# Optimization experiments

Measured on AMD Instinct MI355X. Metric: run time of the kernel, lower is better.

## Reference

```python
import jax, jax.numpy as jnp
import numpy as np

C = 128
K = 5
M = 150000   # num vertices
NF = 300000  # num faces
D = 192      # volume side
NEG_SLOPE = 0.2


def _x_shift(K):
    # Exactly replicates the torch module's grid construction.
    grid = np.linspace(-K // 2, K // 2, K)
    grid_3d = np.stack(np.meshgrid(grid, grid, grid), axis=0).transpose(2, 1, 3, 0)
    return jnp.asarray(grid_3d.reshape(-1, 3), jnp.float32)  # [K^3, 3]


def _trilinear_border(vol, g):
    # vol: [D1, D2, D3]; g: [N, 3] normalized coords in (x, y, z) order
    # (x -> D3/W, y -> D2/H, z -> D1/D), align_corners=True, padding_mode='border'.
    D1, D2, D3 = vol.shape
    def pix(c, S):
        return jnp.clip((c + 1.0) * 0.5 * (S - 1), 0.0, S - 1.0)
    ix, iy, iz = pix(g[:, 0], D3), pix(g[:, 1], D2), pix(g[:, 2], D1)
    x0f, y0f, z0f = jnp.floor(ix), jnp.floor(iy), jnp.floor(iz)
    wx, wy, wz = ix - x0f, iy - y0f, iz - z0f
    x0 = x0f.astype(jnp.int32); y0 = y0f.astype(jnp.int32); z0 = z0f.astype(jnp.int32)
    x1 = jnp.minimum(x0 + 1, D3 - 1)
    y1 = jnp.minimum(y0 + 1, D2 - 1)
    z1 = jnp.minimum(z0 + 1, D1 - 1)
    c000 = vol[z0, y0, x0]; c001 = vol[z0, y0, x1]
    c010 = vol[z0, y1, x0]; c011 = vol[z0, y1, x1]
    c100 = vol[z1, y0, x0]; c101 = vol[z1, y0, x1]
    c110 = vol[z1, y1, x0]; c111 = vol[z1, y1, x1]
    c00 = c000 * (1 - wx) + c001 * wx
    c01 = c010 * (1 - wx) + c011 * wx
    c10 = c100 * (1 - wx) + c101 * wx
    c11 = c110 * (1 - wx) + c111 * wx
    c0 = c00 * (1 - wy) + c01 * wy
    c1 = c10 * (1 - wy) + c11 * wy
    return c0 * (1 - wz) + c1 * wz


def _leaky(x):
    return jnp.where(x >= 0, x, NEG_SLOPE * x)


def setup_inputs() -> dict:
    key = jax.random.key(0)
    ks = jax.random.split(key, 9)
    v = jax.random.uniform(ks[0], (1, M, 3), jnp.float32, -0.9, 0.9)
    f = jax.random.randint(ks[1], (1, NF, 3), 0, M, jnp.int32)
    V = jax.random.normal(ks[2], (1, 1, D, D, D), jnp.float32)
    def init(k, shape, fan):
        return jax.random.normal(k, shape, jnp.float32) / np.sqrt(fan).astype(np.float32)
    Wconv = init(ks[3], (C, 1, K, K, K), K ** 3)
    bconv = jnp.zeros((C,), jnp.float32)
    Wlfc = init(ks[4], (C, C), C)
    blfc = jnp.zeros((C,), jnp.float32)
    W1 = init(ks[5], (C, 6), 6)
    b1 = jnp.zeros((C,), jnp.float32)
    W2 = init(ks[6], (4 * C, 2 * C), 2 * C)
    b2 = jnp.zeros((4 * C,), jnp.float32)
    W3 = init(ks[7], (2 * C, 4 * C), 4 * C)
    b3 = jnp.zeros((2 * C,), jnp.float32)
    return dict(v=v, f=f, V=V, Wconv=Wconv, bconv=bconv, Wlfc=Wlfc, blfc=blfc,
                W1=W1, b1=b1, W2=W2, b2=b2, W3=W3, b3=b3)


def reference(v, f, V, Wconv, bconv, Wlfc, blfc, W1, b1, W2, b2, W3, b3):
    m = v.shape[1]
    D1, D2, D3 = V.shape[2], V.shape[3], V.shape[4]
    Dm = max(D1, D2, D3)
    rescale = jnp.array([D3 / Dm, D2 / Dm, D1 / Dm], jnp.float32)
    x_shift = _x_shift(K)  # [K^3, 3]

    # --- cube sampling (Q = n_scale = 1), done under no_grad in torch ---
    pts = (v[0][:, None, :] + x_shift / Dm * 2.0) / rescale  # [m, K^3, 3]
    cubes = _trilinear_border(V[0, 0], pts.reshape(-1, 3)).reshape(m, K ** 3)
    cubes = jax.lax.stop_gradient(cubes)

    # --- localconv: Conv3d with full-size kernel == GEMM over flattened cube ---
    z_local = cubes @ Wconv.reshape(C, -1).T + bconv      # [m, C]
    z_local = _leaky(z_local)
    z_local = _leaky(z_local @ Wlfc.T + blfc)             # [m, C]

    # --- vertex normals (area-weighted face-normal accumulation, pytorch3d style) ---
    faces = f[0]
    vv = v[0]
    p0, p1, p2 = vv[faces[:, 0]], vv[faces[:, 1]], vv[faces[:, 2]]
    fn = jnp.cross(p1 - p0, p2 - p0)
    vn = jnp.zeros_like(vv)
    vn = vn.at[faces[:, 0]].add(fn).at[faces[:, 1]].add(fn).at[faces[:, 2]].add(fn)
    vn = vn / jnp.maximum(jnp.linalg.norm(vn, axis=-1, keepdims=True), 1e-6)

    # --- point-wise MLP fusion ---
    x = jnp.concatenate([v, vn[None]], axis=2)            # [1, m, 6]
    z_point = _leaky(x @ W1.T + b1)                       # [1, m, C]
    z = jnp.concatenate([z_point, z_local[None]], axis=2) # [1, m, 2C]
    z = _leaky(z @ W2.T + b2)                             # [1, m, 4C]
    z = _leaky(z @ W3.T + b3)                             # [1, m, 2C]
    return z
```

## Files before the change

kernel.cpp:

```cpp
#include <hip/hip_runtime.h>
#include <hip/hip_fp16.h>

#define NEG_SLOPE 0.2f

using f16x8 = __attribute__((ext_vector_type(8))) _Float16;
using f32x4 = __attribute__((ext_vector_type(4))) float;

__device__ __forceinline__ float leakyf(float x) { return x >= 0.f ? x : NEG_SLOPE * x; }

__device__ __forceinline__ void gload_lds16(const void* g, void* l) {
    __builtin_amdgcn_global_load_lds(
        (const __attribute__((address_space(1))) unsigned int*)g,
        (__attribute__((address_space(3))) unsigned int*)l, 16, 0, 0);
}

#define MFMA16(a, b, c) __builtin_amdgcn_mfma_f32_16x16x32_f16(a, b, c, 0, 0, 0)

__global__ __launch_bounds__(256)
void fn_kernel(const float* __restrict__ v, const int* __restrict__ f,
               float4* __restrict__ fn4, int nf) {
    int i = blockIdx.x * 256 + threadIdx.x;
    if (i >= nf) return;
    int i0 = f[3 * i], i1 = f[3 * i + 1], i2 = f[3 * i + 2];
    float p0x = v[3 * i0], p0y = v[3 * i0 + 1], p0z = v[3 * i0 + 2];
    float ux = v[3 * i1] - p0x, uy = v[3 * i1 + 1] - p0y, uz = v[3 * i1 + 2] - p0z;
    float wx = v[3 * i2] - p0x, wy = v[3 * i2 + 1] - p0y, wz = v[3 * i2 + 2] - p0z;
    fn4[i] = make_float4(uy * wz - uz * wy, uz * wx - ux * wz, ux * wy - uy * wx, 0.f);
}

__global__ __launch_bounds__(256)
void inc_hist_kernel(const int* __restrict__ f, unsigned* __restrict__ gh, int NE) {
    __shared__ unsigned h[1024];
    const int t = threadIdx.x, blk = blockIdx.x;
    h[t] = 0; h[t + 256] = 0; h[t + 512] = 0; h[t + 768] = 0;
    __syncthreads();
    int base = blk * 4096;
#pragma unroll
    for (int k = 0; k < 16; ++k) {
        int idx = base + k * 256 + t;
        if (idx < NE) atomicAdd(&h[((unsigned)f[idx]) >> 8], 1u);
    }
    __syncthreads();
#pragma unroll
    for (int k = 0; k < 4; ++k) { int b = t + k * 256; gh[(size_t)blk * 1024 + b] = h[b]; }
}

__global__ __launch_bounds__(256)
void row_scan_kernel(unsigned* __restrict__ gh, unsigned* __restrict__ binTotals, int NB) {
    __shared__ unsigned s[256];
    __shared__ unsigned carrySh;
    const int bin = blockIdx.x, t = threadIdx.x;
    if (t == 0) carrySh = 0;
    __syncthreads();
    for (int base = 0; base < NB; base += 256) {
        unsigned c = carrySh;
        int i = base + t;
        unsigned val = (i < NB) ? gh[(size_t)i * 1024 + bin] : 0;
        s[t] = val;
        __syncthreads();
        for (int d = 1; d < 256; d <<= 1) {
            unsigned x = (t >= d) ? s[t - d] : 0;
            __syncthreads();
            s[t] += x;
            __syncthreads();
        }
        if (i < NB) gh[(size_t)i * 1024 + bin] = s[t] - val + c;
        if (t == 255) carrySh = c + s[255];
        __syncthreads();
    }
    if (t == 0) binTotals[bin] = carrySh;
}

__global__ __launch_bounds__(1024)
void bin_scan_kernel(const unsigned* __restrict__ binTotals, unsigned* __restrict__ binstart) {
    __shared__ unsigned s[1024];
    int t = threadIdx.x;
    unsigned val = binTotals[t];
    s[t] = val;
    __syncthreads();
    for (int d = 1; d < 1024; d <<= 1) {
        unsigned x = (t >= d) ? s[t - d] : 0;
        __syncthreads();
        s[t] += x;
        __syncthreads();
    }
    binstart[t] = s[t] - val;
    if (t == 1023) binstart[1024] = s[1023];
}

__global__ __launch_bounds__(256)
void inc_scatter_kernel(const int* __restrict__ f, const unsigned* __restrict__ gh,
                        const unsigned* __restrict__ binstart,
                        unsigned* __restrict__ sortedV, unsigned* __restrict__ sortedE,
                        int NE) {
    __shared__ unsigned loc[1024];
    const int t = threadIdx.x, blk = blockIdx.x;
#pragma unroll
    for (int k = 0; k < 4; ++k) {
        int b = t + k * 256;
        loc[b] = gh[(size_t)blk * 1024 + b] + binstart[b];
    }
    __syncthreads();
    int base = blk * 4096;
#pragma unroll
    for (int k = 0; k < 16; ++k) {
        int idx = base + k * 256 + t;
        if (idx < NE) {
            unsigned vv = (unsigned)f[idx];
            unsigned pos = atomicAdd(&loc[vv >> 8], 1u);
            sortedV[pos] = vv;
            sortedE[pos] = (unsigned)idx;
        }
    }
}

__global__ __launch_bounds__(256)
void vn_gather_kernel(const unsigned* __restrict__ sortedV, const unsigned* __restrict__ sortedE,
                      const float4* __restrict__ fn4, const unsigned* __restrict__ binstart,
                      float* __restrict__ vn, int M) {
    __shared__ float acc[768];
    const int t = threadIdx.x, b = blockIdx.x;
    acc[t] = 0.f; acc[t + 256] = 0.f; acc[t + 512] = 0.f;
    __syncthreads();
    unsigned s = binstart[b], e = binstart[b + 1];
    for (unsigned i = s + t; i < e; i += 256) {
        unsigned vv = sortedV[i];
        float4 fn = fn4[sortedE[i] / 3];
        int lv = (int)(vv & 255u) * 3;
        atomicAdd(&acc[lv + 0], fn.x);
        atomicAdd(&acc[lv + 1], fn.y);
        atomicAdd(&acc[lv + 2], fn.z);
    }
    __syncthreads();
    int gv = b * 256 + t;
    if (gv < M) {
        vn[3 * gv + 0] = acc[t * 3 + 0];
        vn[3 * gv + 1] = acc[t * 3 + 1];
        vn[3 * gv + 2] = acc[t * 3 + 2];
    }
}

__global__ __launch_bounds__(256)
void code_hist_kernel(const float* __restrict__ v, int* __restrict__ codes,
                      int* __restrict__ hist, int M) {
    int i = blockIdx.x * 256 + threadIdx.x;
    if (i >= M) return;
    int cx = min(max((int)((v[3 * i + 0] + 1.f) * 8.f), 0), 15);
    int cy = min(max((int)((v[3 * i + 1] + 1.f) * 8.f), 0), 15);
    int cz = min(max((int)((v[3 * i + 2] + 1.f) * 8.f), 0), 15);
    int code = 0;
#pragma unroll
    for (int b = 0; b < 4; ++b)
        code |= (((cx >> b) & 1) << (3 * b)) | (((cy >> b) & 1) << (3 * b + 1)) |
                (((cz >> b) & 1) << (3 * b + 2));
    codes[i] = code;
    atomicAdd(&hist[code], 1);
}

__global__ __launch_bounds__(1024)
void scan_kernel(const int* __restrict__ hist, int* __restrict__ offs) {
    __shared__ int s[1024];
    int t = threadIdx.x;
    int v0 = hist[4 * t], v1 = hist[4 * t + 1], v2 = hist[4 * t + 2], v3 = hist[4 * t + 3];
    int sum = v0 + v1 + v2 + v3;
    s[t] = sum;
    __syncthreads();
    for (int d = 1; d < 1024; d <<= 1) {
        int val = (t >= d) ? s[t - d] : 0;
        __syncthreads();
        s[t] += val;
        __syncthreads();
    }
    int excl = s[t] - sum;
    offs[4 * t + 0] = excl;
    offs[4 * t + 1] = excl + v0;
    offs[4 * t + 2] = excl + v0 + v1;
    offs[4 * t + 3] = excl + v0 + v1 + v2;
}

__global__ __launch_bounds__(256)
void scatter_kernel(const int* __restrict__ codes, int* __restrict__ offs,
                    int* __restrict__ perm, int M) {
    int i = blockIdx.x * 256 + threadIdx.x;
    if (i >= M) return;
    int pos = atomicAdd(&offs[codes[i]], 1);
    perm[pos] = i;
}

__global__ __launch_bounds__(256)
void sample_kernel(const float* __restrict__ v, const float* __restrict__ vol,
                   const int* __restrict__ perm,
                   __half* __restrict__ cubes, int m_start, int cnt, int nwg) {
    __shared__ float bbox[2][448];
    __shared__ int pi0[2][16];
    __shared__ float pw[2][16];
    const int half = threadIdx.x >> 7;
    const int q = threadIdx.x & 127;
    int q8 = nwg >> 3, r8 = nwg & 7;
    int xcd = blockIdx.x & 7, idxb = blockIdx.x >> 3;
    int bid = (xcd < r8 ? xcd * (q8 + 1) : r8 * (q8 + 1) + (xcd - r8) * q8) + idxb;
    int ml = bid * 2 + half;
    bool valid = ml < cnt;
    int m = valid ? perm[m_start + ml] : 0;

    if (valid && q < 15) {
        int axis = q / 5, idx = q - 5 * axis;
        float g = -3.f + 1.25f * (float)idx;
        float p = v[3 * m + axis] + g / 192.f * 2.f;
        float pos = fminf(fmaxf((p + 1.f) * 0.5f * 191.f, 0.f), 191.f);
        float fl = floorf(pos);
        pi0[half][q] = (int)fl;
        pw[half][q] = pos - fl;
    }
    __syncthreads();
    if (valid) {
        int xlo = pi0[half][0], ylo = pi0[half][5], zlo = pi0[half][10];
        int j = q & 63;
        int dy = j >> 3, dx = j & 7;
        if (dy < 7) {
            int X = min(xlo + dx, 191);
            int Y = min(ylo + dy, 191);
            int rowoff = dy * 9 + dx;
            const float* volYX = vol + Y * 192 + X;
#pragma unroll
            for (int k = 0; k < 4; ++k) {
                int pz = (q >> 6) + k * 2;
                if (pz < 7) {
                    int Z = min(zlo + pz, 191);
                    bbox[half][pz * 63 + rowoff] = volYX[Z * 36864];
                }
            }
        }
    }
    __syncthreads();
    if (!valid) return;
    __half* dst = cubes + (size_t)ml * 128;
    if (q >= 125) { dst[q] = __float2half(0.f); return; }
    int a = q % 5, b = (q / 5) % 5, c = q / 25;
    int xlo = pi0[half][0], ylo = pi0[half][5], zlo = pi0[half][10];
    int gx0 = pi0[half][a], gy0 = pi0[half][5 + b], gz0 = pi0[half][10 + c];
    float wxv = pw[half][a], wyv = pw[half][5 + b], wzv = pw[half][10 + c];
    int x0 = gx0 - xlo, y0 = gy0 - ylo, z0 = gz0 - zlo;
    int x1 = min(gx0 + 1, 191) - xlo;
    int y1 = min(gy0 + 1, 191) - ylo;
    int z1 = min(gz0 + 1, 191) - zlo;
    const float* bb = bbox[half];
    int b00 = z0 * 63 + y0 * 9, b01 = z0 * 63 + y1 * 9;
    int b10 = z1 * 63 + y0 * 9, b11 = z1 * 63 + y1 * 9;
    float c000 = bb[b00 + x0], c001 = bb[b00 + x1];
    float c010 = bb[b01 + x0], c011 = bb[b01 + x1];
    float c100 = bb[b10 + x0], c101 = bb[b10 + x1];
    float c110 = bb[b11 + x0], c111 = bb[b11 + x1];
    float omx = 1.f - wxv, omy = 1.f - wyv, omz = 1.f - wzv;
    float c00 = c000 * omx + c001 * wxv;
    float c01 = c010 * omx + c011 * wxv;
    float c10 = c100 * omx + c101 * wxv;
    float c11 = c110 * omx + c111 * wxv;
    float c0 = c00 * omy + c01 * wyv;
    float c1 = c10 * omy + c11 * wyv;
    dst[25 * a + 5 * b + c] = __float2half(c0 * omz + c1 * wzv);
}

__global__ __launch_bounds__(256)
void prep_weights(const float* __restrict__ Wconv, const float* __restrict__ Wlfc,
                  const float* __restrict__ W2, const float* __restrict__ W3,
                  __half* __restrict__ wpadh, __half* __restrict__ wlfch,
                  __half* __restrict__ w2h, __half* __restrict__ w3h) {
    int b = blockIdx.x, t = threadIdx.x;
    if (b < 64) {
        int i = b * 256 + t; int ch = i >> 7, k = i & 127;
        wpadh[i] = __float2half(k < 125 ? Wconv[ch * 125 + k] : 0.f);
    } else if (b < 128) {
        int i = (b - 64) * 256 + t; wlfch[i] = __float2half(Wlfc[i]);
    } else if (b < 640) {
        int i = (b - 128) * 256 + t; w2h[i] = __float2half(W2[i]);
    } else {
        int i = (b - 640) * 256 + t; w3h[i] = __float2half(W3[i]);
    }
}

__global__ __launch_bounds__(256)
void point_kernel(const float* __restrict__ v, const float* __restrict__ vn,
                  const int* __restrict__ perm,
                  const float* __restrict__ W1, const float* __restrict__ b1,
                  __half* __restrict__ zcat, int m_start, int cnt) {
    int ml = blockIdx.x * 2 + (threadIdx.x >> 7);
    if (ml >= cnt) return;
    int n = threadIdx.x & 127;
    int m = perm[m_start + ml];
    float x0 = v[3 * m], x1 = v[3 * m + 1], x2 = v[3 * m + 2];
    float nx = vn[3 * m], ny = vn[3 * m + 1], nz = vn[3 * m + 2];
    float nrm = fmaxf(sqrtf(nx * nx + ny * ny + nz * nz), 1e-6f);
    nx /= nrm; ny /= nrm; nz /= nrm;
    const float* w = W1 + n * 6;
    float z = b1[n] + x0 * w[0] + x1 * w[1] + x2 * w[2] + nx * w[3] + ny * w[4] + nz * w[5];
    zcat[(size_t)ml * 256 + n] = __float2half(leakyf(z));
}

__global__ __launch_bounds__(256)
void convlfc_kernel(const __half* __restrict__ cubes, const __half* __restrict__ wconvh,
                    const float* __restrict__ bconv, const __half* __restrict__ wlfch,
                    const float* __restrict__ blfc, __half* __restrict__ zcat) {
    __shared__ __half Zt[128 * 128];
    __shared__ __half As[128 * 64];
    __shared__ __half Bs[128 * 64];
    const int t = threadIdx.x;
    const int lane = t & 63, wave = t >> 6;
    const int lr = lane & 15, lg = lane >> 4;
    const int wm = wave >> 1, wn = wave & 1;
    const int m0 = blockIdx.x * 128;
    const int srow = t >> 3;
    const int scb = ((t & 7) << 4) ^ (((t >> 3) & 7) << 4);
    const int swz = (lr & 7) << 4;

    const __half* Ag = cubes + (size_t)(m0 + srow) * 128 + (scb >> 1);
    const __half* Bg = wconvh + (size_t)srow * 128 + (scb >> 1);
    __half* Al = As + wave * 512;
    __half* Bl = Bs + wave * 512;
    const char* aB = (const char*)As + (wm * 64 + lr) * 128;
    const char* bB = (const char*)Bs + (wn * 64 + lr) * 128;

    f32x4 acc[4][4] = {};
    for (int kc = 0; kc < 128; kc += 64) {
#pragma unroll
        for (int i = 0; i < 4; ++i) {
            gload_lds16(Ag + (size_t)i * 32 * 128 + kc, Al + i * 2048);
            gload_lds16(Bg + (size_t)i * 32 * 128 + kc, Bl + i * 2048);
        }
        __syncthreads();
#pragma unroll
        for (int kk = 0; kk < 2; ++kk) {
            const int ko = (kk * 64 + lg * 16) ^ swz;
            f16x8 af[4], bf[4];
#pragma unroll
            for (int fx = 0; fx < 4; ++fx) {
                af[fx] = *(const f16x8*)(aB + fx * 2048 + ko);
                bf[fx] = *(const f16x8*)(bB + fx * 2048 + ko);
            }
#pragma unroll
            for (int fm = 0; fm < 4; ++fm)
#pragma unroll
                for (int fn = 0; fn < 4; ++fn)
                    acc[fm][fn] = MFMA16(af[fm], bf[fn], acc[fm][fn]);
        }
        __syncthreads();
    }
#pragma unroll
    for (int fm = 0; fm < 4; ++fm) {
#pragma unroll
        for (int fn = 0; fn < 4; ++fn) {
            int col = wn * 64 + fn * 16 + lr;
            float bias = bconv[col];
#pragma unroll
            for (int r = 0; r < 4; ++r) {
                int row = wm * 64 + fm * 16 + lg * 4 + r;
                float val = leakyf(acc[fm][fn][r] + bias);
                *(__half*)((char*)Zt + row * 256 + ((2 * col) ^ ((row & 7) << 4))) = __float2half(val);
            }
        }
    }
    __syncthreads();

    const __half* Bg2 = wlfch + (size_t)srow * 128 + (scb >> 1);
    const char* zR = (const char*)Zt + (wm * 64 + lr) * 256;
    f32x4 acc2[4][4] = {};
    for (int kc = 0; kc < 128; kc += 64) {
#pragma unroll
        for (int i = 0; i < 4; ++i)
            gload_lds16(Bg2 + (size_t)i * 32 * 128 + kc, Bl + i * 2048);
        __syncthreads();
#pragma unroll
        for (int kk = 0; kk < 2; ++kk) {
            const int kb = kc * 2 + kk * 64 + lg * 16;
            const int ko = (kk * 64 + lg * 16) ^ swz;
            f16x8 af[4], bf[4];
#pragma unroll
            for (int fx = 0; fx < 4; ++fx) {
                af[fx] = *(const f16x8*)(zR + fx * 4096 + (kb ^ swz));
                bf[fx] = *(const f16x8*)(bB + fx * 2048 + ko);
            }
#pragma unroll
            for (int fm = 0; fm < 4; ++fm)
#pragma unroll
                for (int fn = 0; fn < 4; ++fn)
                    acc2[fm][fn] = MFMA16(af[fm], bf[fn], acc2[fm][fn]);
        }
        __syncthreads();
    }
#pragma unroll
    for (int fm = 0; fm < 4; ++fm) {
#pragma unroll
        for (int fn = 0; fn < 4; ++fn) {
            int col = wn * 64 + fn * 16 + lr;
            float bias = blfc[col];
#pragma unroll
            for (int r = 0; r < 4; ++r) {
                int row = m0 + wm * 64 + fm * 16 + lg * 4 + r;
                zcat[(size_t)row * 256 + 128 + col] = __float2half(leakyf(acc2[fm][fn][r] + bias));
            }
        }
    }
}

template<bool F32OUT>
__global__ __launch_bounds__(256)
void gemm_wide(const __half* __restrict__ A, const __half* __restrict__ W,
               const float* __restrict__ bias, void* __restrict__ outp,
               int K, int Meff, int OS, int OC, const int* __restrict__ rowmap) {
    __shared__ __half As[2][4096];
    __shared__ __half Bs[2][16384];
    const int t = threadIdx.x;
    const int lane = t & 63, wave = t >> 6;
    const int lr = lane & 15, lg = lane >> 4;
    const int m0 = blockIdx.x * 64, n0 = blockIdx.y * 256;

    const int srow = t >> 3;
    const int scb = ((t & 7) << 4) ^ (((t >> 3) & 7) << 4);
    const __half* Ag = A + (size_t)(m0 + srow) * K + (scb >> 1);
    const __half* Wg = W + (size_t)(n0 + srow) * K + (scb >> 1);

    const int swz = (lr & 7) << 4;
    const int aOff = lr * 128;
    const int bOff = (wave * 64 + lr) * 128;
    const int k0 = (lg * 16) ^ swz;
    const int k1 = (64 + lg * 16) ^ swz;

    f32x4 acc[4][4] = {};

    {
        __half* Al = As[0] + wave * 512;
        __half* Bl = Bs[0] + wave * 512;
#pragma unroll
        for (int i = 0; i < 2; ++i)
            gload_lds16(Ag + (size_t)i * 32 * K, Al + i * 2048);
#pragma unroll
        for (int i = 0; i < 8; ++i)
            gload_lds16(Wg + (size_t)i * 32 * K, Bl + i * 2048);
    }
    __syncthreads();

    int cur = 0;
    for (int kc = 0; kc < K; kc += 64) {
        if (kc + 64 < K) {
            __half* Al = As[cur ^ 1] + wave * 512;
            __half* Bl = Bs[cur ^ 1] + wave * 512;
#pragma unroll
            for (int i = 0; i < 2; ++i)
                gload_lds16(Ag + (size_t)i * 32 * K + kc + 64, Al + i * 2048);
#pragma unroll
            for (int i = 0; i < 8; ++i)
                gload_lds16(Wg + (size_t)i * 32 * K + kc + 64, Bl + i * 2048);
        }
        const char* aB = (const char*)As[cur] + aOff;
        const char* bB = (const char*)Bs[cur] + bOff;
        f16x8 af[4], bf[4];
#pragma unroll
        for (int fx = 0; fx < 4; ++fx) {
            af[fx] = *(const f16x8*)(aB + fx * 2048 + k0);
            bf[fx] = *(const f16x8*)(bB + fx * 2048 + k0);
        }
#pragma unroll
        for (int fm = 0; fm < 4; ++fm)
#pragma unroll
            for (int fn = 0; fn < 4; ++fn)
                acc[fm][fn] = MFMA16(af[fm], bf[fn], acc[fm][fn]);
#pragma unroll
        for (int fx = 0; fx < 4; ++fx) {
            af[fx] = *(const f16x8*)(aB + fx * 2048 + k1);
            bf[fx] = *(const f16x8*)(bB + fx * 2048 + k1);
        }
#pragma unroll
        for (int fm = 0; fm < 4; ++fm)
#pragma unroll
            for (int fn = 0; fn < 4; ++fn)
                acc[fm][fn] = MFMA16(af[fm], bf[fn], acc[fm][fn]);
        __syncthreads();
        cur ^= 1;
    }

    float bv[4];
#pragma unroll
    for (int fn = 0; fn < 4; ++fn) bv[fn] = bias[n0 + wave * 64 + fn * 16 + lr];
    const int rbase = m0 + lg * 4;
    const int cbase = OC + n0 + wave * 64 + lr;
#pragma unroll
    for (int fm = 0; fm < 4; ++fm) {
#pragma unroll
        for (int r = 0; r < 4; ++r) {
            int row = rbase + fm * 16 + r;
            if (row < Meff) {
                size_t orow = (size_t)(rowmap ? rowmap[row] : row);
#pragma unroll
                for (int fn = 0; fn < 4; ++fn) {
                    float val = leakyf(acc[fm][fn][r] + bv[fn]);
                    if (F32OUT)
                        ((float*)outp)[orow * OS + cbase + fn * 16] = val;
                    else
                        ((__half*)outp)[orow * OS + cbase + fn * 16] = __float2half(val);
                }
            }
        }
    }
}

extern "C" void kernel_launch(void* const* d_in, const int* in_sizes, int n_in,
                              void* d_out, int out_size, void* d_ws, size_t ws_size,
                              hipStream_t stream) {
    const float* v = (const float*)d_in[0];
    const int* f = (const int*)d_in[1];
    const float* vol = (const float*)d_in[2];
    const float* Wconv = (const float*)d_in[3];
    const float* bconv = (const float*)d_in[4];
    const float* Wlfc = (const float*)d_in[5];
    const float* blfc = (const float*)d_in[6];
    const float* W1 = (const float*)d_in[7];
    const float* b1 = (const float*)d_in[8];
    const float* W2 = (const float*)d_in[9];
    const float* b2 = (const float*)d_in[10];
    const float* W3 = (const float*)d_in[11];
    const float* b3 = (const float*)d_in[12];
    float* out = (float*)d_out;
    const int M = in_sizes[0] / 3;
    const int NF = in_sizes[1] / 3;
    const int NE = 3 * NF;
    const int NB = (NE + 4095) / 4096;

    char* base = (char*)d_ws;
    float* vn = (float*)base;
    size_t off = ((size_t)M * 12 + 255) & ~(size_t)255;
    int* codes = (int*)(base + off); off += ((size_t)M * 4 + 255) & ~(size_t)255;
    int* perm  = (int*)(base + off); off += ((size_t)M * 4 + 255) & ~(size_t)255;
    int* hist  = (int*)(base + off); off += 4096 * 4;
    int* offs  = (int*)(base + off); off += 4096 * 4;
    float4* fn4 = (float4*)(base + off); off += (size_t)NF * 16;
    unsigned* sortedV = (unsigned*)(base + off); off += ((size_t)NE * 4 + 255) & ~(size_t)255;
    unsigned* sortedE = (unsigned*)(base + off); off += ((size_t)NE * 4 + 255) & ~(size_t)255;
    unsigned* gh = (unsigned*)(base + off); off += ((size_t)1024 * NB * 4 + 255) & ~(size_t)255;
    unsigned* binstart = (unsigned*)(base + off); off += 1032 * 4;
    unsigned* binTotals = (unsigned*)(base + off); off += 1024 * 4;
    __half* wpadh = (__half*)(base + off); off += 32768;
    __half* wlfch = (__half*)(base + off); off += 32768;
    __half* w2h = (__half*)(base + off); off += 262144;
    __half* w3h = (__half*)(base + off); off += 262144;
    size_t avail = ws_size > off ? ws_size - off : 0;
    size_t Mpad = ((size_t)M + 127) & ~(size_t)127;
    size_t chm = (avail / 1792) & ~(size_t)127;
    if (chm > Mpad) chm = Mpad;
    if (chm < 128) chm = 128;
    __half* cubes = (__half*)(base + off);
    __half* zcat = cubes + chm * 128;
    __half* h = zcat + chm * 256;

    fn_kernel<<<(NF + 255) / 256, 256, 0, stream>>>(v, f, fn4, NF);
    inc_hist_kernel<<<NB, 256, 0, stream>>>(f, gh, NE);
    row_scan_kernel<<<1024, 256, 0, stream>>>(gh, binTotals, NB);
    bin_scan_kernel<<<1, 1024, 0, stream>>>(binTotals, binstart);
    inc_scatter_kernel<<<NB, 256, 0, stream>>>(f, gh, binstart, sortedV, sortedE, NE);
    vn_gather_kernel<<<(M + 255) / 256, 256, 0, stream>>>(sortedV, sortedE, fn4, binstart, vn, M);

    hipMemsetAsync(hist, 0, 4096 * 4, stream);
    code_hist_kernel<<<(M + 255) / 256, 256, 0, stream>>>(v, codes, hist, M);
    scan_kernel<<<1, 1024, 0, stream>>>(hist, offs);
    scatter_kernel<<<(M + 255) / 256, 256, 0, stream>>>(codes, offs, perm, M);
    prep_weights<<<1152, 256, 0, stream>>>(Wconv, Wlfc, W2, W3, wpadh, wlfch, w2h, w3h);

    for (size_t ms = 0; ms < (size_t)M; ms += chm) {
        size_t rem = (size_t)M - ms;
        int cnt = (int)(rem < chm ? rem : chm);
        int mb = (cnt + 127) / 128;
        int mb64 = (cnt + 63) / 64;
        int nblk = (cnt + 1) / 2;
        sample_kernel<<<nblk, 256, 0, stream>>>(v, vol, perm, cubes, (int)ms, cnt, nblk);
        convlfc_kernel<<<mb, 256, 0, stream>>>(cubes, wpadh, bconv, wlfch, blfc, zcat);
        point_kernel<<<(cnt + 1) / 2, 256, 0, stream>>>(v, vn, perm, W1, b1, zcat, (int)ms, cnt);
        gemm_wide<false><<<dim3(mb64, 2), 256, 0, stream>>>(zcat, w2h, b2, h, 256, mb64 * 64, 512, 0, nullptr);
        gemm_wide<true><<<dim3(mb64, 1), 256, 0, stream>>>(h, w3h, b3, out, 512, cnt, 256, 0, perm + ms);
    }
}
```

Baseline: 504.8 us.

## Make MLP GEMMs persistent with LDS-resident weight slices

Replaces the wide GEMM kernel with a persistent-style kernel. Each block loads its full 128-column weight slice (all of K) into LDS once, then loops over 128-row M tiles with a grid-stride loop. A 2x2 wave tiling replaces the 1x4 layout. The goal is to stop re-streaming weights from global memory for every 64-row tile and to cut launch-grid overhead. In exchange it uses much more LDS per block (64KB for W2, 128KB plus A buffers for W3), which limits occupancy, and single-buffered A loads in the first GEMM expose load latency.

```diff
diff --git a/kernel.cpp b/kernel.cpp
--- a/kernel.cpp
+++ b/kernel.cpp
@@ -402,101 +402,113 @@
     }
 }
 
-template<bool F32OUT>
-__global__ __launch_bounds__(256)
-void gemm_wide(const __half* __restrict__ A, const __half* __restrict__ W,
-               const float* __restrict__ bias, void* __restrict__ outp,
-               int K, int Meff, int OS, int OC, const int* __restrict__ rowmap) {
-    __shared__ __half As[2][4096];
-    __shared__ __half Bs[2][16384];
+template<int KT, bool DBUF, bool F32OUT>
+__global__ __launch_bounds__(256)
+void gemm_ws(const __half* __restrict__ A, const __half* __restrict__ W,
+             const float* __restrict__ bias, void* __restrict__ outp,
+             int Mtiles, int Meff, int OS, int OC, const int* __restrict__ rowmap) {
+    __shared__ __half Bs[KT * 8192];
+    __shared__ __half As[(DBUF ? 2 : 1) * 8192];
+    const int K = KT * 64;
     const int t = threadIdx.x;
     const int lane = t & 63, wave = t >> 6;
     const int lr = lane & 15, lg = lane >> 4;
-    const int m0 = blockIdx.x * 64, n0 = blockIdx.y * 256;
-
+    const int wm = wave >> 1, wn = wave & 1;
+    const int n0 = blockIdx.y * 128;
     const int srow = t >> 3;
     const int scb = ((t & 7) << 4) ^ (((t >> 3) & 7) << 4);
-    const __half* Ag = A + (size_t)(m0 + srow) * K + (scb >> 1);
-    const __half* Wg = W + (size_t)(n0 + srow) * K + (scb >> 1);
-
     const int swz = (lr & 7) << 4;
-    const int aOff = lr * 128;
-    const int bOff = (wave * 64 + lr) * 128;
+
+    {
+        const __half* Wg = W + (size_t)(n0 + srow) * K + (scb >> 1);
+        __half* Bl = Bs + wave * 512;
+#pragma unroll
+        for (int kt = 0; kt < KT; ++kt)
+#pragma unroll
+            for (int i = 0; i < 4; ++i)
+                gload_lds16(Wg + (size_t)i * 32 * K + kt * 64, Bl + kt * 8192 + i * 2048);
+    }
+
+    const int aOff = (wm * 64 + lr) * 128;
+    const int bOff = (wn * 64 + lr) * 128;
     const int k0 = (lg * 16) ^ swz;
     const int k1 = (64 + lg * 16) ^ swz;
 
-    f32x4 acc[4][4] = {};
-
-    {
-        __half* Al = As[0] + wave * 512;
-        __half* Bl = Bs[0] + wave * 512;
-#pragma unroll
-        for (int i = 0; i < 2; ++i)
-            gload_lds16(Ag + (size_t)i * 32 * K, Al + i * 2048);
-#pragma unroll
-        for (int i = 0; i < 8; ++i)
-            gload_lds16(Wg + (size_t)i * 32 * K, Bl + i * 2048);
-    }
-    __syncthreads();
-
-    int cur = 0;
-    for (int kc = 0; kc < K; kc += 64) {
-        if (kc + 64 < K) {
-            __half* Al = As[cur ^ 1] + wave * 512;
-            __half* Bl = Bs[cur ^ 1] + wave * 512;
-#pragma unroll
-            for (int i = 0; i < 2; ++i)
-                gload_lds16(Ag + (size_t)i * 32 * K + kc + 64, Al + i * 2048);
-#pragma unroll
-            for (int i = 0; i < 8; ++i)
-                gload_lds16(Wg + (size_t)i * 32 * K + kc + 64, Bl + i * 2048);
-        }
-        const char* aB = (const char*)As[cur] + aOff;
-        const char* bB = (const char*)Bs[cur] + bOff;
-        f16x8 af[4], bf[4];
-#pragma unroll
-        for (int fx = 0; fx < 4; ++fx) {
-            af[fx] = *(const f16x8*)(aB + fx * 2048 + k0);
-            bf[fx] = *(const f16x8*)(bB + fx * 2048 + k0);
-        }
-#pragma unroll
-        for (int fm = 0; fm < 4; ++fm)
-#pragma unroll
-            for (int fn = 0; fn < 4; ++fn)
-                acc[fm][fn] = MFMA16(af[fm], bf[fn], acc[fm][fn]);
-#pragma unroll
-        for (int fx = 0; fx < 4; ++fx) {
-            af[fx] = *(const f16x8*)(aB + fx * 2048 + k1);
-            bf[fx] = *(const f16x8*)(bB + fx * 2048 + k1);
-        }
-#pragma unroll
-        for (int fm = 0; fm < 4; ++fm)
-#pragma unroll
-            for (int fn = 0; fn < 4; ++fn)
-                acc[fm][fn] = MFMA16(af[fm], bf[fn], acc[fm][fn]);
-        __syncthreads();
-        cur ^= 1;
-    }
-
     float bv[4];
 #pragma unroll
-    for (int fn = 0; fn < 4; ++fn) bv[fn] = bias[n0 + wave * 64 + fn * 16 + lr];
-    const int rbase = m0 + lg * 4;
-    const int cbase = OC + n0 + wave * 64 + lr;
-#pragma unroll
-    for (int fm = 0; fm < 4; ++fm) {
-#pragma unroll
-        for (int r = 0; r < 4; ++r) {
-            int row = rbase + fm * 16 + r;
-            if (row < Meff) {
-                size_t orow = (size_t)(rowmap ? rowmap[row] : row);
-#pragma unroll
-                for (int fn = 0; fn < 4; ++fn) {
-                    float val = leakyf(acc[fm][fn][r] + bv[fn]);
-                    if (F32OUT)
-                        ((float*)outp)[orow * OS + cbase + fn * 16] = val;
-                    else
-                        ((__half*)outp)[orow * OS + cbase + fn * 16] = __float2half(val);
+    for (int fn = 0; fn < 4; ++fn) bv[fn] = bias[n0 + wn * 64 + fn * 16 + lr];
+
+    for (int mt = blockIdx.x; mt < Mtiles; mt += gridDim.x) {
+        const int m0 = mt * 128;
+        const __half* Ag = A + (size_t)(m0 + srow) * K + (scb >> 1);
+        f32x4 acc[4][4] = {};
+        {
+            __half* Al = As + wave * 512;
+#pragma unroll
+            for (int i = 0; i < 4; ++i)
+                gload_lds16(Ag + (size_t)i * 32 * K, Al + i * 2048);
+        }
+        __syncthreads();
+        int cur = 0;
+#pragma unroll
+        for (int kt = 0; kt < KT; ++kt) {
+            if (DBUF && kt + 1 < KT) {
+                __half* Al = As + (cur ^ 1) * 8192 + wave * 512;
+#pragma unroll
+                for (int i = 0; i < 4; ++i)
+                    gload_lds16(Ag + (size_t)i * 32 * K + (kt + 1) * 64, Al + i * 2048);
+            }
+            const char* aB = (const char*)As + cur * 16384 + aOff;
+            const char* bT = (const char*)Bs + kt * 16384 + bOff;
+            f16x8 af[4], bf[4];
+#pragma unroll
+            for (int fx = 0; fx < 4; ++fx) {
+                af[fx] = *(const f16x8*)(aB + fx * 2048 + k0);
+                bf[fx] = *(const f16x8*)(bT + fx * 2048 + k0);
+            }
+#pragma unroll
+            for (int fm = 0; fm < 4; ++fm)
+#pragma unroll
+                for (int fn = 0; fn < 4; ++fn)
+                    acc[fm][fn] = MFMA16(af[fm], bf[fn], acc[fm][fn]);
+#pragma unroll
+            for (int fx = 0; fx < 4; ++fx) {
+                af[fx] = *(const f16x8*)(aB + fx * 2048 + k1);
+                bf[fx] = *(const f16x8*)(bT + fx * 2048 + k1);
+            }
+#pragma unroll
+            for (int fm = 0; fm < 4; ++fm)
+#pragma unroll
+                for (int fn = 0; fn < 4; ++fn)
+                    acc[fm][fn] = MFMA16(af[fm], bf[fn], acc[fm][fn]);
+            if (!DBUF && kt + 1 < KT) {
+                __syncthreads();
+                __half* Al = As + wave * 512;
+#pragma unroll
+                for (int i = 0; i < 4; ++i)
+                    gload_lds16(Ag + (size_t)i * 32 * K + (kt + 1) * 64, Al + i * 2048);
+            }
+            __syncthreads();
+            if (DBUF) cur ^= 1;
+        }
+
+        const int rbase = m0 + wm * 64 + lg * 4;
+        const int cbase = OC + n0 + wn * 64 + lr;
+#pragma unroll
+        for (int fm = 0; fm < 4; ++fm) {
+#pragma unroll
+            for (int r = 0; r < 4; ++r) {
+                int row = rbase + fm * 16 + r;
+                if (row < Meff) {
+                    size_t orow = (size_t)(rowmap ? rowmap[row] : row);
+#pragma unroll
+                    for (int fn = 0; fn < 4; ++fn) {
+                        float val = leakyf(acc[fm][fn][r] + bv[fn]);
+                        if (F32OUT)
+                            ((float*)outp)[orow * OS + cbase + fn * 16] = val;
+                        else
+                            ((__half*)outp)[orow * OS + cbase + fn * 16] = __float2half(val);
+                    }
                 }
             }
         }
@@ -568,12 +580,13 @@
         size_t rem = (size_t)M - ms;
         int cnt = (int)(rem < chm ? rem : chm);
         int mb = (cnt + 127) / 128;
-        int mb64 = (cnt + 63) / 64;
         int nblk = (cnt + 1) / 2;
         sample_kernel<<<nblk, 256, 0, stream>>>(v, vol, perm, cubes, (int)ms, cnt, nblk);
         convlfc_kernel<<<mb, 256, 0, stream>>>(cubes, wpadh, bconv, wlfch, blfc, zcat);
         point_kernel<<<(cnt + 1) / 2, 256, 0, stream>>>(v, vn, perm, W1, b1, zcat, (int)ms, cnt);
-        gemm_wide<false><<<dim3(mb64, 2), 256, 0, stream>>>(zcat, w2h, b2, h, 256, mb64 * 64, 512, 0, nullptr);
-        gemm_wide<true><<<dim3(mb64, 1), 256, 0, stream>>>(h, w3h, b3, out, 512, cnt, 256, 0, perm + ms);
-    }
-}
+        gemm_ws<4, false, false><<<dim3(256, 4), 256, 0, stream>>>(
+            zcat, w2h, b2, h, mb, mb * 128, 512, 0, nullptr);
+        gemm_ws<8, true, true><<<dim3(256, 2), 256, 0, stream>>>(
+            h, w3h, b3, out, mb, cnt, 256, 0, perm + ms);
+    }
+}
```

New measurement: 510.2 us. About the same (+1.1%).

## Replace LDS-staged wide GEMMs with register-direct global-load MFMA GEMMs

Applied to the files above, without the earlier changes.

The two MLP GEMMs (256->512 and 512->256) no longer stage A and W tiles through double-buffered shared memory with global_load_lds and barriers. Each wave instead loads its MFMA fragments straight from global memory into registers, with K fixed at compile time and the loop fully unrolled, and launch bounds request 4 blocks per CU. This removes LDS traffic and synchronisation and raises occupancy. In exchange, A rows are fetched redundantly by all four waves, the global loads are strided and uncoalesced, and without software prefetch the kernel depends on caches and occupancy to hide latency.

```diff
diff --git a/kernel.cpp b/kernel.cpp
--- a/kernel.cpp
+++ b/kernel.cpp
@@ -402,87 +402,47 @@
     }
 }
 
-template<bool F32OUT>
-__global__ __launch_bounds__(256)
-void gemm_wide(const __half* __restrict__ A, const __half* __restrict__ W,
-               const float* __restrict__ bias, void* __restrict__ outp,
-               int K, int Meff, int OS, int OC, const int* __restrict__ rowmap) {
-    __shared__ __half As[2][4096];
-    __shared__ __half Bs[2][16384];
+template<int KT, bool F32OUT>
+__global__ __launch_bounds__(256, 4)
+void gemm_reg(const __half* __restrict__ A, const __half* __restrict__ W,
+              const float* __restrict__ bias, void* __restrict__ outp,
+              int Meff, int OS, int OC, const int* __restrict__ rowmap) {
+    const int K = KT * 64;
     const int t = threadIdx.x;
     const int lane = t & 63, wave = t >> 6;
     const int lr = lane & 15, lg = lane >> 4;
-    const int m0 = blockIdx.x * 64, n0 = blockIdx.y * 256;
-
-    const int srow = t >> 3;
-    const int scb = ((t & 7) << 4) ^ (((t >> 3) & 7) << 4);
-    const __half* Ag = A + (size_t)(m0 + srow) * K + (scb >> 1);
-    const __half* Wg = W + (size_t)(n0 + srow) * K + (scb >> 1);
-
-    const int swz = (lr & 7) << 4;
-    const int aOff = lr * 128;
-    const int bOff = (wave * 64 + lr) * 128;
-    const int k0 = (lg * 16) ^ swz;
-    const int k1 = (64 + lg * 16) ^ swz;
+    const int m0 = blockIdx.x * 64;
+    const int c0 = blockIdx.y * 256 + wave * 64;
+
+    const __half* Ab = A + (size_t)(m0 + lr) * K + lg * 8;
+    const __half* Bb = W + (size_t)(c0 + lr) * K + lg * 8;
 
     f32x4 acc[4][4] = {};
-
-    {
-        __half* Al = As[0] + wave * 512;
-        __half* Bl = Bs[0] + wave * 512;
-#pragma unroll
-        for (int i = 0; i < 2; ++i)
-            gload_lds16(Ag + (size_t)i * 32 * K, Al + i * 2048);
-#pragma unroll
-        for (int i = 0; i < 8; ++i)
-            gload_lds16(Wg + (size_t)i * 32 * K, Bl + i * 2048);
-    }
-    __syncthreads();
-
-    int cur = 0;
-    for (int kc = 0; kc < K; kc += 64) {
-        if (kc + 64 < K) {
-            __half* Al = As[cur ^ 1] + wave * 512;
-            __half* Bl = Bs[cur ^ 1] + wave * 512;
-#pragma unroll
-            for (int i = 0; i < 2; ++i)
-                gload_lds16(Ag + (size_t)i * 32 * K + kc + 64, Al + i * 2048);
-#pragma unroll
-            for (int i = 0; i < 8; ++i)
-                gload_lds16(Wg + (size_t)i * 32 * K + kc + 64, Bl + i * 2048);
-        }
-        const char* aB = (const char*)As[cur] + aOff;
-        const char* bB = (const char*)Bs[cur] + bOff;
-        f16x8 af[4], bf[4];
-#pragma unroll
-        for (int fx = 0; fx < 4; ++fx) {
-            af[fx] = *(const f16x8*)(aB + fx * 2048 + k0);
-            bf[fx] = *(const f16x8*)(bB + fx * 2048 + k0);
-        }
-#pragma unroll
-        for (int fm = 0; fm < 4; ++fm)
+#pragma unroll
+    for (int kt = 0; kt < KT; ++kt) {
+#pragma unroll
+        for (int kk = 0; kk < 2; ++kk) {
+            const int ko = kt * 64 + kk * 32;
+            f16x8 af[4], bf[4];
+#pragma unroll
+            for (int fm = 0; fm < 4; ++fm)
+                af[fm] = *(const f16x8*)(Ab + (size_t)fm * 16 * K + ko);
 #pragma unroll
             for (int fn = 0; fn < 4; ++fn)
-                acc[fm][fn] = MFMA16(af[fm], bf[fn], acc[fm][fn]);
-#pragma unroll
-        for (int fx = 0; fx < 4; ++fx) {
-            af[fx] = *(const f16x8*)(aB + fx * 2048 + k1);
-            bf[fx] = *(const f16x8*)(bB + fx * 2048 + k1);
-        }
-#pragma unroll
-        for (int fm = 0; fm < 4; ++fm)
-#pragma unroll
-            for (int fn = 0; fn < 4; ++fn)
-                acc[fm][fn] = MFMA16(af[fm], bf[fn], acc[fm][fn]);
-        __syncthreads();
-        cur ^= 1;
+                bf[fn] = *(const f16x8*)(Bb + (size_t)fn * 16 * K + ko);
+#pragma unroll
+            for (int fm = 0; fm < 4; ++fm)
+#pragma unroll
+                for (int fn = 0; fn < 4; ++fn)
+                    acc[fm][fn] = MFMA16(af[fm], bf[fn], acc[fm][fn]);
+        }
     }
 
     float bv[4];
 #pragma unroll
-    for (int fn = 0; fn < 4; ++fn) bv[fn] = bias[n0 + wave * 64 + fn * 16 + lr];
+    for (int fn = 0; fn < 4; ++fn) bv[fn] = bias[c0 + fn * 16 + lr];
     const int rbase = m0 + lg * 4;
-    const int cbase = OC + n0 + wave * 64 + lr;
+    const int cbase = OC + c0 + lr;
 #pragma unroll
     for (int fm = 0; fm < 4; ++fm) {
 #pragma unroll
@@ -573,7 +533,9 @@
         sample_kernel<<<nblk, 256, 0, stream>>>(v, vol, perm, cubes, (int)ms, cnt, nblk);
         convlfc_kernel<<<mb, 256, 0, stream>>>(cubes, wpadh, bconv, wlfch, blfc, zcat);
         point_kernel<<<(cnt + 1) / 2, 256, 0, stream>>>(v, vn, perm, W1, b1, zcat, (int)ms, cnt);
-        gemm_wide<false><<<dim3(mb64, 2), 256, 0, stream>>>(zcat, w2h, b2, h, 256, mb64 * 64, 512, 0, nullptr);
-        gemm_wide<true><<<dim3(mb64, 1), 256, 0, stream>>>(h, w3h, b3, out, 512, cnt, 256, 0, perm + ms);
-    }
-}
+        gemm_reg<4, false><<<dim3(mb64, 2), 256, 0, stream>>>(
+            zcat, w2h, b2, h, mb64 * 64, 512, 0, nullptr);
+        gemm_reg<8, true><<<dim3(mb64, 1), 256, 0, stream>>>(
+            h, w3h, b3, out, cnt, 256, 0, perm + ms);
+    }
+}
```

Result: slower. 661.6 us (+31.1%).
